# Performance work log

Measured on AMD Instinct MI355X. Metric: run time of the kernel, lower is better.

The kernel has to match this reference:

```python
import jax, jax.numpy as jnp
from jax import lax
import numpy as np

B, N = 2, 1024  # batch of NxN linear-system matrices
DN = ('NCHW', 'OIHW', 'NCHW')


def _conv(x, w, b, pad):
    # cross-correlation, same convention as torch/spconv
    return lax.conv_general_dilated(x, w, (1, 1), pad, dimension_numbers=DN) + b[None, :, None, None]


def _spread_mask(m, pad):
    # regular sparse conv: output site active iff any input site in 2x2 window is active
    ones = jnp.ones((1, 1, 2, 2), dtype=m.dtype)
    return (lax.conv_general_dilated(m, ones, (1, 1), pad, dimension_numbers=DN) > 0).astype(m.dtype)


def _prelu(x, a):
    return jnp.where(x >= 0, x, a * x)


def setup_inputs() -> dict:
    key = jax.random.key(0)
    ks = jax.random.split(key, 10)
    mask = jax.random.randint(ks[0], (B, N, N), 0, 2, dtype=jnp.int32)
    x = jax.random.normal(ks[1], (B, 1, N, N), dtype=jnp.float32)

    def w(k, o, i, kh, kw):
        return jax.random.normal(k, (o, i, kh, kw), dtype=jnp.float32) / np.sqrt(i * kh * kw)

    def bias(k, o):
        return 0.01 * jax.random.normal(k, (o,), dtype=jnp.float32)

    return {
        'x': x, 'mask': mask,
        'w1': w(ks[2], 8, 1, 1, 1), 'b1': bias(ks[6], 8), 'a1': jnp.float32(0.25),
        'w2': w(ks[3], 16, 8, 2, 2), 'b2': bias(ks[7], 16), 'a2': jnp.float32(0.25),
        'w3': w(ks[4], 8, 16, 2, 2), 'b3': bias(ks[8], 8), 'a3': jnp.float32(0.25),
        'w4': w(ks[5], 1, 8, 1, 1), 'b4': bias(ks[9], 1),
    }


def reference(x, mask, w1, b1, a1, w2, b2, a2, w3, b3, a3, w4, b4):
    m = (mask > 0).astype(jnp.float32)[:, None]          # [B,1,N,N] active-site mask
    h = x * m                                            # sparse input: zeros at inactive sites
    # layer 1: 1x1 conv + PReLU (mask unchanged)
    h = _conv(h, w1, b1, ((0, 0), (0, 0))) * m
    h = _prelu(h, a1)
    # layer 2: 2x2 conv, padding (1,0) -> [B,16,N+1,N-1]
    p2 = ((1, 1), (0, 0))
    m2 = _spread_mask(m, p2)
    h = _conv(h, w2, b2, p2) * m2
    h = _prelu(h, a2)
    # layer 3: 2x2 conv, padding (0,1) -> [B,8,N,N]
    p3 = ((0, 0), (1, 1))
    m3 = _spread_mask(m2, p3)
    h = _conv(h, w3, b3, p3) * m3
    h = _prelu(h, a3)
    # layer 4: 1x1 conv (mask unchanged)
    h = _conv(h, w4, b4, ((0, 0), (0, 0))) * m3          # [B,1,N,N]
    # triangular masking on sparse indices (row=indices[:,1], col=indices[:,2])
    row = jnp.arange(N)[:, None]
    col = jnp.arange(N)[None, :]
    h = jnp.where((row >= col)[None, None], h, jnp.float32(0))
    diag_active = (row == col)[None, None] & (m3 > 0)
    h = jnp.where(diag_active, jax.nn.softplus(h), h)
    return h
```

## Files before the change

### kernel.cpp

```cpp
#include <hip/hip_runtime.h>
#include <hip/hip_bf16.h>
#include <math.h>

#define N 1024
#define TB 16

typedef __attribute__((ext_vector_type(8))) short short8;
typedef __attribute__((ext_vector_type(4))) short short4v;
typedef __attribute__((ext_vector_type(4))) float f32x4;

__device__ __forceinline__ float prelu(float v, float a) {
    return fmaxf(v, 0.f) + a * fminf(v, 0.f);
}

__device__ __forceinline__ short f2bf(float f) {
    return (short)__bfloat16_as_ushort(__float2bfloat16(f));
}

__global__ __launch_bounds__(256, 8) void precond_mfma(
    const float* __restrict__ xg, const int* __restrict__ maskg,
    const float* __restrict__ w1, const float* __restrict__ b1, const float* __restrict__ a1p,
    const float* __restrict__ w2, const float* __restrict__ b2, const float* __restrict__ a2p,
    const float* __restrict__ w3, const float* __restrict__ b3, const float* __restrict__ a3p,
    const float* __restrict__ w4, const float* __restrict__ b4p,
    float* __restrict__ out)
{
    const int tid = threadIdx.x;
    const int bz  = blockIdx.z;
    const int t   = blockIdx.x;

    int by = (int)((sqrtf(8.0f * (float)t + 1.0f) - 1.0f) * 0.5f);
    while ((by + 1) * (by + 2) / 2 <= t) ++by;
    while (by * (by + 1) / 2 > t) --by;
    const int bx = t - by * (by + 1) / 2;
    const int ty0 = by * TB, tx0 = bx * TB;

    const int lane = tid & 63, wid = tid >> 6;
    const int c16 = lane & 15, g = lane >> 4;

    const float w2r0 = w2[tid];
    const float w2r1 = w2[tid + 256];
    const float w3r0 = w3[tid];
    const float w3r1 = w3[tid + 256];

    const int pA0 = tid;
    const int pA1 = tid + 256;
    const bool s1valid = (pA1 < 324);
    const bool s1wave  = ((tid - lane) + 256 < 324);
    const int dyA0 = pA0 / 18, dxA0 = pA0 - dyA0 * 18;
    const int dyA1 = pA1 / 18, dxA1 = pA1 - dyA1 * 18;

    int gy0 = ty0 - 1 + dyA0, gx0 = tx0 - 1 + dxA0;
    const bool in0 = (unsigned)gy0 < N && (unsigned)gx0 < N;
    size_t i0 = in0 ? (((size_t)bz * N + gy0) * N + gx0) : 0;
    const int   mr0 = maskg[i0];
    const float xr0 = xg[i0];

    int mr1 = 0; float xr1 = 0.f; bool in1 = false;
    if (s1wave) {
        int gy1 = ty0 - 1 + dyA1, gx1 = tx0 - 1 + dxA1;
        in1 = s1valid && (unsigned)gy1 < N && (unsigned)gx1 < N;
        size_t i1 = in1 ? (((size_t)bz * N + gy1) * N + gx1) : 0;
        mr1 = maskg[i1];
        xr1 = xg[i1];
    }

    if (by < 63) {
        int zy = bx * TB + (tid >> 4), zx = (by + 1) * TB + (tid & 15);
        out[((size_t)bz * N + zy) * N + zx] = 0.f;
    }

    __shared__ __align__(16) short sW2[512];
    __shared__ __align__(16) short sW3h[512];
    __shared__ __align__(16) short h1s[324 * 8];
    __shared__ __align__(16) short h2lo[4][85 * 8];
    __shared__ __align__(16) short h2hi[4][85 * 8];
    __shared__ __align__(16) unsigned RM1[12];

    const float a1 = a1p[0], a2 = a2p[0], a3 = a3p[0];
    const float b4 = b4p[0];
    const bool leftEdge  = (tx0 == 0);
    const bool rightEdge = (tx0 == N - TB);

    {
        int s0 = tid, s1 = tid + 256;
        sW2[(s0 & ~31) | ((s0 & 3) << 3) | ((s0 >> 2) & 7)] = f2bf(w2r0);
        sW2[(s1 & ~31) | ((s1 & 3) << 3) | ((s1 >> 2) & 7)] = f2bf(w2r1);
        sW3h[(s0 & ~63) | ((s0 & 3) << 4) | ((s0 >> 2) & 15)] = f2bf(w3r0);
        sW3h[(s1 & ~63) | ((s1 & 3) << 4) | ((s1 >> 2) & 15)] = f2bf(w3r1);
    }

    {
        bool mb = in0 && (mr0 > 0);
        float xv = in0 ? xr0 : 0.f;
        unsigned long long bal = __ballot(mb);
        if (lane == 0) *(uint2*)&RM1[2 * wid] = make_uint2((unsigned)bal, (unsigned)(bal >> 32));
        short8 hv;
#pragma unroll
        for (int ch = 0; ch < 8; ++ch) hv[ch] = f2bf(prelu(fmaf(xv, w1[ch], b1[ch]), a1));
        if (!mb) hv = (short8)0;
        *(short8*)&h1s[pA0 * 8] = hv;

        if (s1wave) {
            bool mb1 = in1 && (mr1 > 0);
            float xv1 = in1 ? xr1 : 0.f;
            unsigned long long bal1 = __ballot(mb1);
            if (lane == 0) *(uint2*)&RM1[2 * (wid + 4)] = make_uint2((unsigned)bal1, (unsigned)(bal1 >> 32));
            if (s1valid) {
                short8 hv1;
#pragma unroll
                for (int ch = 0; ch < 8; ++ch) hv1[ch] = f2bf(prelu(fmaf(xv1, w1[ch], b1[ch]), a1));
                if (!mb1) hv1 = (short8)0;
                *(short8*)&h1s[pA1 * 8] = hv1;
            }
        }
    }
    __syncthreads();

    unsigned M2w0, M2w1, M2w2;
    {
        short8 a2f = *(const short8*)&sW2[c16 * 32 + g * 8];
        const int kh = g >> 1, kw = g & 1;
        const int rowbase = wid * 4;
        f32x4 bias2;
#pragma unroll
        for (int r = 0; r < 4; ++r) bias2[r] = b2[g * 4 + r];

        unsigned mw[3] = {0, 0, 0};
#pragma unroll
        for (int grp = 0; grp < 6; ++grp) {
            int pl = grp * 16 + c16;
            bool valid = pl < 85;
            int plc = valid ? pl : 84;
            int lr = plc / 17, dx2 = plc - lr * 17;
            int dy2 = rowbase + lr;

            short8 bf = *(const short8*)&h1s[((dy2 + kh) * 18 + dx2 + kw) * 8];
            f32x4 acc = __builtin_amdgcn_mfma_f32_16x16x32_bf16(a2f, bf, bias2, 0, 0, 0);

            int q = dy2 * 18 + dx2, w0 = q >> 5, sh = q & 31;
            unsigned long long v64 = ((unsigned long long)RM1[w0 + 1] << 32) | RM1[w0];
            unsigned long long v = v64 >> sh;
            unsigned m2 = (unsigned)((v | (v >> 1) | (v >> 18) | (v >> 19)) & 1ull);
            if ((leftEdge && dx2 == 0) || (rightEdge && dx2 == 16)) m2 = 0;
            if (!valid) m2 = 0;

            unsigned bits16 = (unsigned)(__ballot(m2 != 0) & 0xFFFFull);
            if (grp == 0) mw[0]  = bits16;
            if (grp == 1) mw[0] |= bits16 << 16;
            if (grp == 2) mw[1]  = bits16;
            if (grp == 3) mw[1] |= bits16 << 16;
            if (grp == 4) mw[2]  = bits16;
            if (grp == 5) mw[2] |= bits16 << 16;

            short4v hv;
#pragma unroll
            for (int r = 0; r < 4; ++r) hv[r] = f2bf(prelu(acc[r], a2));
            if (m2 == 0) { hv[0] = 0; hv[1] = 0; hv[2] = 0; hv[3] = 0; }

            if (valid) {
                short* dst = (g & 2) ? &h2hi[wid][0] : &h2lo[wid][0];
                *(short4v*)&dst[plc * 8 + (g & 1) * 4] = hv;
            }
        }
        M2w0 = mw[0]; M2w1 = mw[1]; M2w2 = mw[2];
    }

    {
        short8 a3f0 = *(const short8*)&sW3h[(c16 & 7) * 64 + g * 8];
        short8 a3f1 = *(const short8*)&sW3h[(c16 & 7) * 64 + 32 + g * 8];
        if (c16 >= 8) { a3f0 = (short8)0; a3f1 = (short8)0; }
        const int kwC = g >> 1, ic8 = g & 1;
        const short* h2sel = ic8 ? &h2hi[wid][0] : &h2lo[wid][0];
        f32x4 bias3;
        float w4r[4];
#pragma unroll
        for (int r = 0; r < 4; ++r) {
            bias3[r] = (g < 2) ? b3[g * 4 + r] : 0.f;
            w4r[r]   = (g < 2) ? w4[g * 4 + r] : 0.f;
        }

        unsigned rm[5];
        rm[0] = M2w0 & 0x1FFFFu;
        rm[1] = (unsigned)((((unsigned long long)M2w1 << 32) | M2w0) >> 17) & 0x1FFFFu;
        rm[2] = (M2w1 >> 2) & 0x1FFFFu;
        rm[3] = (unsigned)((((unsigned long long)M2w2 << 32) | M2w1) >> 19) & 0x1FFFFu;
        rm[4] = (M2w2 >> 4) & 0x1FFFFu;

        short8 bfp = *(const short8*)&h2sel[(c16 + kwC) * 8];
#pragma unroll
        for (int j = 0; j < 4; ++j) {
            short8 bfn = *(const short8*)&h2sel[((j + 1) * 17 + c16 + kwC) * 8];
            f32x4 acc = __builtin_amdgcn_mfma_f32_16x16x32_bf16(a3f0, bfp, bias3, 0, 0, 0);
            acc = __builtin_amdgcn_mfma_f32_16x16x32_bf16(a3f1, bfn, acc, 0, 0, 0);
            bfp = bfn;

            float partial = 0.f;
#pragma unroll
            for (int r = 0; r < 4; ++r) partial = fmaf(prelu(acc[r], a3), w4r[r], partial);
            partial += __shfl_xor(partial, 16, 64);

            if (g == 0) {
                unsigned combined = rm[j] | rm[j + 1];
                unsigned m3 = (combined >> c16) & 3u;

                float outv = m3 ? (partial + b4) : 0.f;
                int y = ty0 + wid * 4 + j, x = tx0 + c16;
                if (y < x) {
                    outv = 0.f;
                } else if (y == x && m3) {
                    outv = fmaxf(outv, 0.f) + log1pf(expf(-fabsf(outv)));
                }
                out[((size_t)bz * N + y) * N + x] = outv;
            }
        }
    }
}

extern "C" void kernel_launch(void* const* d_in, const int* in_sizes, int n_in,
                              void* d_out, int out_size, void* d_ws, size_t ws_size,
                              hipStream_t stream) {
    const float* x    = (const float*)d_in[0];
    const int*   mask = (const int*)  d_in[1];
    const float* w1   = (const float*)d_in[2];
    const float* b1   = (const float*)d_in[3];
    const float* a1   = (const float*)d_in[4];
    const float* w2   = (const float*)d_in[5];
    const float* b2   = (const float*)d_in[6];
    const float* a2   = (const float*)d_in[7];
    const float* w3   = (const float*)d_in[8];
    const float* b3   = (const float*)d_in[9];
    const float* a3   = (const float*)d_in[10];
    const float* w4   = (const float*)d_in[11];
    const float* b4   = (const float*)d_in[12];
    float* out = (float*)d_out;

    dim3 grid(2080, 1, 2);
    precond_mfma<<<grid, 256, 0, stream>>>(x, mask, w1, b1, a1, w2, b2, a2,
                                           w3, b3, a3, w4, b4, out);
}
```

Before: 25.58 us.

## Pack two tiles per 512-thread block and compute layer-2 mask rows with bitwise ops

```diff
diff --git a/kernel.cpp b/kernel.cpp
--- a/kernel.cpp
+++ b/kernel.cpp
@@ -17,7 +17,7 @@
     return (short)__bfloat16_as_ushort(__float2bfloat16(f));
 }
 
-__global__ __launch_bounds__(256, 8) void precond_mfma(
+__global__ __launch_bounds__(512, 8) void precond_mfma(
     const float* __restrict__ xg, const int* __restrict__ maskg,
     const float* __restrict__ w1, const float* __restrict__ b1, const float* __restrict__ a1p,
     const float* __restrict__ w2, const float* __restrict__ b2, const float* __restrict__ a2p,
@@ -25,9 +25,15 @@
     const float* __restrict__ w4, const float* __restrict__ b4p,
     float* __restrict__ out)
 {
-    const int tid = threadIdx.x;
-    const int bz  = blockIdx.z;
-    const int t   = blockIdx.x;
+    const int tid  = threadIdx.x;
+    const int bz   = blockIdx.z;
+    const int h    = tid >> 8;
+    const int tl   = tid & 255;
+    const int lane = tid & 63;
+    const int widh = (tid >> 6) & 3;
+    const int c16  = lane & 15, g = lane >> 4;
+
+    const int t = 2 * blockIdx.x + h;
 
     int by = (int)((sqrtf(8.0f * (float)t + 1.0f) - 1.0f) * 0.5f);
     while ((by + 1) * (by + 2) / 2 <= t) ++by;
@@ -35,18 +41,13 @@
     const int bx = t - by * (by + 1) / 2;
     const int ty0 = by * TB, tx0 = bx * TB;
 
-    const int lane = tid & 63, wid = tid >> 6;
-    const int c16 = lane & 15, g = lane >> 4;
-
-    const float w2r0 = w2[tid];
-    const float w2r1 = w2[tid + 256];
-    const float w3r0 = w3[tid];
-    const float w3r1 = w3[tid + 256];
-
-    const int pA0 = tid;
-    const int pA1 = tid + 256;
+    const float w2r = w2[tid];
+    const float w3r = w3[tid];
+
+    const int pA0 = tl;
+    const int pA1 = tl + 256;
     const bool s1valid = (pA1 < 324);
-    const bool s1wave  = ((tid - lane) + 256 < 324);
+    const bool s1wave  = (widh < 2);
     const int dyA0 = pA0 / 18, dxA0 = pA0 - dyA0 * 18;
     const int dyA1 = pA1 / 18, dxA1 = pA1 - dyA1 * 18;
 
@@ -66,67 +67,91 @@
     }
 
     if (by < 63) {
-        int zy = bx * TB + (tid >> 4), zx = (by + 1) * TB + (tid & 15);
+        int zy = bx * TB + (tl >> 4), zx = (by + 1) * TB + (tl & 15);
         out[((size_t)bz * N + zy) * N + zx] = 0.f;
     }
 
     __shared__ __align__(16) short sW2[512];
     __shared__ __align__(16) short sW3h[512];
-    __shared__ __align__(16) short h1s[324 * 8];
-    __shared__ __align__(16) short h2lo[4][85 * 8];
-    __shared__ __align__(16) short h2hi[4][85 * 8];
-    __shared__ __align__(16) unsigned RM1[12];
+    __shared__ __align__(16) short h1s[2][324 * 8];
+    __shared__ __align__(16) short h2lo[2][4][85 * 8];
+    __shared__ __align__(16) short h2hi[2][4][85 * 8];
+    __shared__ unsigned RM1[2][12];
 
     const float a1 = a1p[0], a2 = a2p[0], a3 = a3p[0];
     const float b4 = b4p[0];
     const bool leftEdge  = (tx0 == 0);
     const bool rightEdge = (tx0 == N - TB);
 
-    {
-        int s0 = tid, s1 = tid + 256;
-        sW2[(s0 & ~31) | ((s0 & 3) << 3) | ((s0 >> 2) & 7)] = f2bf(w2r0);
-        sW2[(s1 & ~31) | ((s1 & 3) << 3) | ((s1 >> 2) & 7)] = f2bf(w2r1);
-        sW3h[(s0 & ~63) | ((s0 & 3) << 4) | ((s0 >> 2) & 15)] = f2bf(w3r0);
-        sW3h[(s1 & ~63) | ((s1 & 3) << 4) | ((s1 >> 2) & 15)] = f2bf(w3r1);
-    }
+    sW2[(tid & ~31) | ((tid & 3) << 3) | ((tid >> 2) & 7)] = f2bf(w2r);
+    sW3h[(tid & ~63) | ((tid & 3) << 4) | ((tid >> 2) & 15)] = f2bf(w3r);
 
     {
         bool mb = in0 && (mr0 > 0);
         float xv = in0 ? xr0 : 0.f;
         unsigned long long bal = __ballot(mb);
-        if (lane == 0) *(uint2*)&RM1[2 * wid] = make_uint2((unsigned)bal, (unsigned)(bal >> 32));
+        if (lane == 0) *(uint2*)&RM1[h][2 * widh] =
+            make_uint2((unsigned)bal, (unsigned)(bal >> 32));
         short8 hv;
 #pragma unroll
         for (int ch = 0; ch < 8; ++ch) hv[ch] = f2bf(prelu(fmaf(xv, w1[ch], b1[ch]), a1));
         if (!mb) hv = (short8)0;
-        *(short8*)&h1s[pA0 * 8] = hv;
+        *(short8*)&h1s[h][pA0 * 8] = hv;
 
         if (s1wave) {
             bool mb1 = in1 && (mr1 > 0);
             float xv1 = in1 ? xr1 : 0.f;
             unsigned long long bal1 = __ballot(mb1);
-            if (lane == 0) *(uint2*)&RM1[2 * (wid + 4)] = make_uint2((unsigned)bal1, (unsigned)(bal1 >> 32));
+            if (lane == 0) *(uint2*)&RM1[h][2 * (widh + 4)] =
+                make_uint2((unsigned)bal1, (unsigned)(bal1 >> 32));
             if (s1valid) {
                 short8 hv1;
 #pragma unroll
                 for (int ch = 0; ch < 8; ++ch) hv1[ch] = f2bf(prelu(fmaf(xv1, w1[ch], b1[ch]), a1));
                 if (!mb1) hv1 = (short8)0;
-                *(short8*)&h1s[pA1 * 8] = hv1;
+                *(short8*)&h1s[h][pA1 * 8] = hv1;
             }
         }
     }
     __syncthreads();
 
-    unsigned M2w0, M2w1, M2w2;
+    unsigned m2row[5];
+    {
+        const int bitbase = 72 * widh;
+        unsigned rr[6];
+#pragma unroll
+        for (int i = 0; i < 6; ++i) {
+            int bit = bitbase + 18 * i;
+            int w = bit >> 5, sh = bit & 31;
+            unsigned long long v = ((unsigned long long)RM1[h][w + 1] << 32) | RM1[h][w];
+            rr[i] = (unsigned)(v >> sh);
+        }
+#pragma unroll
+        for (int i = 0; i < 5; ++i) {
+            unsigned u = rr[i] | rr[i + 1];
+            m2row[i] = (u | (u >> 1)) & 0x1FFFFu;
+        }
+        if (leftEdge) {
+#pragma unroll
+            for (int i = 0; i < 5; ++i) m2row[i] &= ~1u;
+        }
+        if (rightEdge) {
+#pragma unroll
+            for (int i = 0; i < 5; ++i) m2row[i] &= ~(1u << 16);
+        }
+    }
+    unsigned M2w0 = m2row[0] | (m2row[1] << 17);
+    unsigned M2w1 = (m2row[1] >> 15) | (m2row[2] << 2) | (m2row[3] << 19);
+    unsigned M2w2 = (m2row[3] >> 13) | (m2row[4] << 4);
+
     {
         short8 a2f = *(const short8*)&sW2[c16 * 32 + g * 8];
         const int kh = g >> 1, kw = g & 1;
-        const int rowbase = wid * 4;
+        const int rowbase = widh * 4;
         f32x4 bias2;
 #pragma unroll
         for (int r = 0; r < 4; ++r) bias2[r] = b2[g * 4 + r];
 
-        unsigned mw[3] = {0, 0, 0};
 #pragma unroll
         for (int grp = 0; grp < 6; ++grp) {
             int pl = grp * 16 + c16;
@@ -135,23 +160,11 @@
             int lr = plc / 17, dx2 = plc - lr * 17;
             int dy2 = rowbase + lr;
 
-            short8 bf = *(const short8*)&h1s[((dy2 + kh) * 18 + dx2 + kw) * 8];
+            short8 bf = *(const short8*)&h1s[h][((dy2 + kh) * 18 + dx2 + kw) * 8];
             f32x4 acc = __builtin_amdgcn_mfma_f32_16x16x32_bf16(a2f, bf, bias2, 0, 0, 0);
 
-            int q = dy2 * 18 + dx2, w0 = q >> 5, sh = q & 31;
-            unsigned long long v64 = ((unsigned long long)RM1[w0 + 1] << 32) | RM1[w0];
-            unsigned long long v = v64 >> sh;
-            unsigned m2 = (unsigned)((v | (v >> 1) | (v >> 18) | (v >> 19)) & 1ull);
-            if ((leftEdge && dx2 == 0) || (rightEdge && dx2 == 16)) m2 = 0;
-            if (!valid) m2 = 0;
-
-            unsigned bits16 = (unsigned)(__ballot(m2 != 0) & 0xFFFFull);
-            if (grp == 0) mw[0]  = bits16;
-            if (grp == 1) mw[0] |= bits16 << 16;
-            if (grp == 2) mw[1]  = bits16;
-            if (grp == 3) mw[1] |= bits16 << 16;
-            if (grp == 4) mw[2]  = bits16;
-            if (grp == 5) mw[2] |= bits16 << 16;
+            unsigned word = (grp < 2) ? M2w0 : ((grp < 4) ? M2w1 : M2w2);
+            unsigned m2 = (word >> (c16 + ((grp & 1) << 4))) & 1u;
 
             short4v hv;
 #pragma unroll
@@ -159,11 +172,10 @@
             if (m2 == 0) { hv[0] = 0; hv[1] = 0; hv[2] = 0; hv[3] = 0; }
 
             if (valid) {
-                short* dst = (g & 2) ? &h2hi[wid][0] : &h2lo[wid][0];
+                short* dst = (g & 2) ? &h2hi[h][widh][0] : &h2lo[h][widh][0];
                 *(short4v*)&dst[plc * 8 + (g & 1) * 4] = hv;
             }
         }
-        M2w0 = mw[0]; M2w1 = mw[1]; M2w2 = mw[2];
     }
 
     {
@@ -171,7 +183,7 @@
         short8 a3f1 = *(const short8*)&sW3h[(c16 & 7) * 64 + 32 + g * 8];
         if (c16 >= 8) { a3f0 = (short8)0; a3f1 = (short8)0; }
         const int kwC = g >> 1, ic8 = g & 1;
-        const short* h2sel = ic8 ? &h2hi[wid][0] : &h2lo[wid][0];
+        const short* h2sel = ic8 ? &h2hi[h][widh][0] : &h2lo[h][widh][0];
         f32x4 bias3;
         float w4r[4];
 #pragma unroll
@@ -179,13 +191,6 @@
             bias3[r] = (g < 2) ? b3[g * 4 + r] : 0.f;
             w4r[r]   = (g < 2) ? w4[g * 4 + r] : 0.f;
         }
-
-        unsigned rm[5];
-        rm[0] = M2w0 & 0x1FFFFu;
-        rm[1] = (unsigned)((((unsigned long long)M2w1 << 32) | M2w0) >> 17) & 0x1FFFFu;
-        rm[2] = (M2w1 >> 2) & 0x1FFFFu;
-        rm[3] = (unsigned)((((unsigned long long)M2w2 << 32) | M2w1) >> 19) & 0x1FFFFu;
-        rm[4] = (M2w2 >> 4) & 0x1FFFFu;
 
         short8 bfp = *(const short8*)&h2sel[(c16 + kwC) * 8];
 #pragma unroll
@@ -201,11 +206,11 @@
             partial += __shfl_xor(partial, 16, 64);
 
             if (g == 0) {
-                unsigned combined = rm[j] | rm[j + 1];
+                unsigned combined = m2row[j] | m2row[j + 1];
                 unsigned m3 = (combined >> c16) & 3u;
 
                 float outv = m3 ? (partial + b4) : 0.f;
-                int y = ty0 + wid * 4 + j, x = tx0 + c16;
+                int y = ty0 + widh * 4 + j, x = tx0 + c16;
                 if (y < x) {
                     outv = 0.f;
                 } else if (y == x && m3) {
@@ -235,7 +240,7 @@
     const float* b4   = (const float*)d_in[12];
     float* out = (float*)d_out;
 
-    dim3 grid(2080, 1, 2);
-    precond_mfma<<<grid, 256, 0, stream>>>(x, mask, w1, b1, a1, w2, b2, a2,
+    dim3 grid(1040, 1, 2);
+    precond_mfma<<<grid, 512, 0, stream>>>(x, mask, w1, b1, a1, w2, b2, a2,
                                            w3, b3, a3, w4, b4, out);
 }
```

Result: no change. 25.37 us (-0.8%).
